# Kernel tuning notes

Measured on AMD Instinct MI355X. Metric: run time of the kernel, lower is better.

Reference implementation:

```python
import jax, jax.numpy as jnp
import numpy as np

N, IN_DIM, OUT_DIM = 8192, 512, 256
ALPHA = 0.2  # LeakyReLU negative slope
MASK_VAL = -9e15


def setup_inputs() -> dict:
    key = jax.random.key(0)
    k1, k2, k3, k4 = jax.random.split(key, 4)
    inp = jax.random.normal(k1, (N, IN_DIM), dtype=jnp.float32)
    adj = jax.random.randint(k2, (N, N), 0, 2, dtype=jnp.int32)
    # xavier-ish scaled params
    weight = jax.random.normal(k3, (IN_DIM, OUT_DIM), dtype=jnp.float32) * (2.0 / (IN_DIM + OUT_DIM)) ** 0.5
    a = jax.random.normal(k4, (2 * OUT_DIM, 1), dtype=jnp.float32) * (2.0 / (2 * OUT_DIM + 1)) ** 0.5
    return {"input": inp, "adj": adj, "weight": weight, "a": a}


def reference(input, adj, weight, a):
    Wh = input @ weight                        # [N, D_out]
    Wh1 = Wh @ a[:OUT_DIM, :]                  # [N, 1]
    Wh2 = Wh @ a[OUT_DIM:, :]                  # [N, 1]
    e = Wh1 + Wh2.T                            # [N, N] broadcast additive score
    e = jnp.where(e > 0, e, ALPHA * e)         # LeakyReLU
    e = jnp.where(adj > 0, e, MASK_VAL)        # adjacency mask
    attention = jax.nn.softmax(e, axis=-1)     # [N, N]
    # dropout p=0.0 -> identity
    out = attention @ Wh                       # [N, D_out]
    return jax.nn.elu(out)
```

## Files before the change

### kernel.cpp

```cpp
#include <hip/hip_runtime.h>
#include <hip/hip_bf16.h>
#include <stdint.h>

#define NN 8192
#define DIN 512
#define DOUT 256
#define NSPLIT 8
#define STRIP (NN / NSPLIT)
#define NSTEP (STRIP / 32)
#define LOG2E 1.4426950408889634f

typedef short short8 __attribute__((ext_vector_type(8)));
typedef float floatx4 __attribute__((ext_vector_type(4)));

__device__ __forceinline__ unsigned short f2bf_rne(float x) {
  unsigned u = __float_as_uint(x);
  u += 0x7fffu + ((u >> 16) & 1u);
  return (unsigned short)(u >> 16);
}

__device__ __forceinline__ unsigned cvt_pk_bf16(float lo, float hi) {
  unsigned r;
  asm("v_cvt_pk_bf16_f32 %0, %1, %2" : "=v"(r) : "v"(lo), "v"(hi));
  return r;
}

__global__ __launch_bounds__(256) void kt_transpose(const float* __restrict__ Wg,
                                                    unsigned short* __restrict__ WT) {
  __shared__ unsigned short sm[32][33];
  int tid = threadIdx.x;
  int bk = blockIdx.x >> 3;
  int bn = blockIdx.x & 7;
  int k0 = bk * 32, n0 = bn * 32;
  int r = tid >> 3, c4 = (tid & 7) * 4;
  const float* src = Wg + (size_t)(k0 + r) * DOUT + n0 + c4;
#pragma unroll
  for (int x = 0; x < 4; ++x) sm[r][c4 + x] = f2bf_rne(src[x]);
  __syncthreads();
  unsigned short* dst = WT + (size_t)(n0 + r) * DIN + k0 + c4;
#pragma unroll
  for (int x = 0; x < 4; ++x) dst[x] = sm[c4 + x][r];
}

__global__ __launch_bounds__(256) void kt_cvtx(const float* __restrict__ X,
                                               unsigned short* __restrict__ Xb) {
  int g = blockIdx.x * 256 + threadIdx.x;
  const float4* p = (const float4*)(X + (size_t)g * 8);
  float4 a = p[0], b = p[1];
  union { unsigned u[4]; short8 s8; } r;
  r.u[0] = cvt_pk_bf16(a.x, a.y);
  r.u[1] = cvt_pk_bf16(a.z, a.w);
  r.u[2] = cvt_pk_bf16(b.x, b.y);
  r.u[3] = cvt_pk_bf16(b.z, b.w);
  *(short8*)(Xb + (size_t)g * 8) = r.s8;
}

__global__ __launch_bounds__(256) void kt_gemm1(const unsigned short* __restrict__ Xb,
                                                const unsigned short* __restrict__ WT,
                                                const float* __restrict__ Ab,
                                                unsigned short* __restrict__ WhT,
                                                float* __restrict__ Wh1,
                                                float* __restrict__ Wh2) {
  int tid = threadIdx.x;
  int w = tid >> 6, lane = tid & 63;
  int col = lane & 15, q = lane >> 4;
  int ib = blockIdx.x & 127;
  int db = blockIdx.x >> 7;
  int i0 = ib * 64;
  int drow = db * 64 + w * 16 + col;
  const unsigned short* abase = WT + (size_t)drow * DIN + q * 8;
  const unsigned short* xbase = Xb + (size_t)(i0 + col) * DIN + q * 8;
  floatx4 acc[4];
#pragma unroll
  for (int t = 0; t < 4; ++t) acc[t] = (floatx4)(0.0f);
  for (int k0 = 0; k0 < DIN; k0 += 32) {
    short8 af = *(const short8*)(abase + k0);
#pragma unroll
    for (int t = 0; t < 4; ++t) {
      short8 bf = *(const short8*)(xbase + (size_t)t * 16 * DIN + k0);
      acc[t] = __builtin_amdgcn_mfma_f32_16x16x32_bf16(af, bf, acc[t], 0, 0, 0);
    }
  }
  int dq = db * 64 + w * 16 + q * 4;
  float a1v[4], a2v[4];
#pragma unroll
  for (int r = 0; r < 4; ++r) {
    a1v[r] = Ab[dq + r] * LOG2E;
    a2v[r] = Ab[DOUT + dq + r] * LOG2E;
  }
#pragma unroll
  for (int t = 0; t < 4; ++t) {
    floatx4 v = acc[t];
    int icol = i0 + t * 16 + col;
#pragma unroll
    for (int r = 0; r < 4; ++r) WhT[(size_t)(dq + r) * NN + icol] = f2bf_rne(v[r]);
    float p1 = v[0] * a1v[0] + v[1] * a1v[1] + v[2] * a1v[2] + v[3] * a1v[3];
    float p2 = v[0] * a2v[0] + v[1] * a2v[1] + v[2] * a2v[2] + v[3] * a2v[3];
    p1 += __shfl_xor(p1, 16);
    p1 += __shfl_xor(p1, 32);
    p2 += __shfl_xor(p2, 16);
    p2 += __shfl_xor(p2, 32);
    if (q == 0) {
      atomicAdd(&Wh1[icol], p1);
      atomicAdd(&Wh2[icol], p2);
    }
  }
}

__device__ __forceinline__ short8 build_a(int4 pa, int4 pb, float wh1, floatx4 w2a,
                                          floatx4 w2b, float& lsum) {
  int av[8] = {pa.x, pa.y, pa.z, pa.w, pb.x, pb.y, pb.z, pb.w};
  float w2[8] = {w2a[0], w2a[1], w2a[2], w2a[3], w2b[0], w2b[1], w2b[2], w2b[3]};
  float wv[8];
#pragma unroll
  for (int e = 0; e < 8; ++e) {
    float sc = wh1 + w2[e];
    sc = fmaxf(sc, 0.2f * sc);
    float ex = __builtin_amdgcn_exp2f(sc);
    wv[e] = (av[e] != 0) ? ex : 0.0f;
  }
  union { unsigned u[4]; short8 s8; } r;
#pragma unroll
  for (int p = 0; p < 4; ++p) {
    unsigned pk = cvt_pk_bf16(wv[2 * p], wv[2 * p + 1]);
    r.u[p] = pk;
    lsum += __uint_as_float(pk << 16) + __uint_as_float(pk & 0xffff0000u);
  }
  return r.s8;
}

__global__ __launch_bounds__(256, 2) void kt_attn(const int* __restrict__ adj,
                                                  const unsigned short* __restrict__ WhT,
                                                  const float* __restrict__ Wh1,
                                                  const float* __restrict__ Wh2,
                                                  float* __restrict__ accg,
                                                  float* __restrict__ lg) {
  __shared__ __align__(16) unsigned short tileB[2][DOUT * 32];
  int tid = threadIdx.x;
  int w = tid >> 6, lane = tid & 63;
  int col = lane & 15, q = lane >> 4;
  int s = blockIdx.x & (NSPLIT - 1);
  int ib = blockIdx.x >> 3;
  int i0 = ib * 128;
  int jb = s * STRIP;

  int r0 = i0 + w * 32 + col;
  float wh1r0 = Wh1[r0];
  float wh1r1 = Wh1[r0 + 16];

  int fsw = (tid >> 1) & 3;
  const unsigned short* gsrc = WhT + (size_t)tid * NN + jb;
  unsigned short* lrow0 = &tileB[0][tid * 32];

  int fc = (col >> 1) & 3;
  const unsigned short* bb0 = &tileB[0][col * 32 + ((q ^ fc) * 8)];

  const int* aptr0 = adj + ((size_t)r0 << 13) + jb + q * 8;
  const int* aptr1 = adj + ((size_t)(r0 + 16) << 13) + jb + q * 8;
  const float* wp = Wh2 + jb + q * 8;

  floatx4 acc0[16], acc1[16];
#pragma unroll
  for (int t = 0; t < 16; ++t) {
    acc0[t] = (floatx4)(0.0f);
    acc1[t] = (floatx4)(0.0f);
  }
  float lp0 = 0.f, lp1 = 0.f;

  short8 st[4];
#pragma unroll
  for (int m = 0; m < 4; ++m) st[m] = *(const short8*)(gsrc + m * 8);
  int4 a0a = *(const int4*)aptr0;
  int4 a0b = *(const int4*)(aptr0 + 4);
  int4 a1a = *(const int4*)aptr1;
  int4 a1b = *(const int4*)(aptr1 + 4);
  floatx4 w2a = *(const floatx4*)wp;
  floatx4 w2b = *(const floatx4*)(wp + 4);

#pragma unroll 1
  for (int k = 0; k < NSTEP; ++k) {
    int bsel = (k & 1) * (DOUT * 32);
    unsigned short* lw = lrow0 + bsel;
#pragma unroll
    for (int m = 0; m < 4; ++m) *(short8*)(lw + ((m ^ fsw) * 8)) = st[m];
    __syncthreads();
    if (k + 1 < NSTEP) {
      const unsigned short* gs = gsrc + (size_t)(k + 1) * 32;
#pragma unroll
      for (int m = 0; m < 4; ++m) st[m] = *(const short8*)(gs + m * 8);
    }
    short8 af0 = build_a(a0a, a0b, wh1r0, w2a, w2b, lp0);
    short8 af1 = build_a(a1a, a1b, wh1r1, w2a, w2b, lp1);
    if (k + 1 < NSTEP) {
      int jn = (k + 1) * 32;
      a0a = *(const int4*)(aptr0 + jn);
      a0b = *(const int4*)(aptr0 + jn + 4);
      a1a = *(const int4*)(aptr1 + jn);
      a1b = *(const int4*)(aptr1 + jn + 4);
      w2a = *(const floatx4*)(wp + jn);
      w2b = *(const floatx4*)(wp + jn + 4);
    }
    const unsigned short* br = bb0 + bsel;
#pragma unroll
    for (int h = 0; h < 4; ++h) {
      short8 bf[4];
#pragma unroll
      for (int t = 0; t < 4; ++t) bf[t] = *(const short8*)(br + (h * 4 + t) * 512);
#pragma unroll
      for (int t = 0; t < 4; ++t) {
        acc0[h * 4 + t] =
            __builtin_amdgcn_mfma_f32_16x16x32_bf16(af0, bf[t], acc0[h * 4 + t], 0, 0, 0);
        acc1[h * 4 + t] =
            __builtin_amdgcn_mfma_f32_16x16x32_bf16(af1, bf[t], acc1[h * 4 + t], 0, 0, 0);
      }
    }
  }

  lp0 += __shfl_xor(lp0, 16);
  lp0 += __shfl_xor(lp0, 32);
  lp1 += __shfl_xor(lp1, 16);
  lp1 += __shfl_xor(lp1, 32);
  if (lane < 16) {
    atomicAdd(&lg[i0 + w * 32 + lane], lp0);
    atomicAdd(&lg[i0 + w * 32 + 16 + lane], lp1);
  }
#pragma unroll
  for (int T = 0; T < 16; ++T) {
    floatx4 v0 = acc0[T];
    floatx4 v1 = acc1[T];
    int dcol = T * 16 + col;
    int irow0 = i0 + w * 32 + q * 4;
#pragma unroll
    for (int r = 0; r < 4; ++r) atomicAdd(&accg[(size_t)(irow0 + r) * DOUT + dcol], v0[r]);
#pragma unroll
    for (int r = 0; r < 4; ++r)
      atomicAdd(&accg[(size_t)(irow0 + 16 + r) * DOUT + dcol], v1[r]);
  }
}

__global__ __launch_bounds__(256) void kt_merge(const float* __restrict__ accg,
                                                const float* __restrict__ lg,
                                                float* __restrict__ out) {
  int g = blockIdx.x * 256 + threadIdx.x;
  int i = g >> 6;
  float inv = 1.0f / lg[i];
  float4 v = *(const float4*)(accg + (size_t)g * 4);
  float o[4] = {v.x * inv, v.y * inv, v.z * inv, v.w * inv};
#pragma unroll
  for (int r = 0; r < 4; ++r) o[r] = o[r] > 0.f ? o[r] : (__expf(o[r]) - 1.f);
  *(float4*)(out + (size_t)g * 4) = make_float4(o[0], o[1], o[2], o[3]);
}

extern "C" void kernel_launch(void* const* d_in, const int* in_sizes, int n_in,
                              void* d_out, int out_size, void* d_ws, size_t ws_size,
                              hipStream_t stream) {
  const float* X = (const float*)d_in[0];
  const int* adj = (const int*)d_in[1];
  const float* Wg = (const float*)d_in[2];
  const float* Ab = (const float*)d_in[3];
  float* out = (float*)d_out;

  char* ws = (char*)d_ws;
  float* accg = (float*)ws;
  unsigned short* Xb = (unsigned short*)ws;
  size_t off = (size_t)NN * DOUT * 4;
  float* lg = (float*)(ws + off);
  off += (size_t)NN * 4;
  float* Wh1 = (float*)(ws + off);
  off += (size_t)NN * 4;
  float* Wh2 = (float*)(ws + off);
  off += (size_t)NN * 4;
  unsigned short* WT = (unsigned short*)(ws + off);
  off += (size_t)DOUT * DIN * 2;
  unsigned short* WhT = (unsigned short*)(ws + off);
  off += (size_t)DOUT * NN * 2;

  hipMemsetAsync(Wh1, 0, (size_t)NN * 8, stream);
  kt_cvtx<<<2048, 256, 0, stream>>>(X, Xb);
  kt_transpose<<<128, 256, 0, stream>>>(Wg, WT);
  kt_gemm1<<<512, 256, 0, stream>>>(Xb, WT, Ab, WhT, Wh1, Wh2);
  hipMemsetAsync(ws, 0, (size_t)NN * DOUT * 4 + (size_t)NN * 4, stream);
  kt_attn<<<(NN / 128) * NSPLIT, 256, 0, stream>>>(adj, WhT, Wh1, Wh2, accg, lg);
  kt_merge<<<2048, 256, 0, stream>>>(accg, lg, out);
}
```

Measured before the change: 471.0 us.

## Load Wh B-fragments directly from global, drop LDS staging, nontemporal adj loads

Removes the double-buffered shared-memory tile for WhT and the per-step __syncthreads. Each wave now loads its 16 B fragments straight from global memory, relying on L2/L1 to serve the four waves that share them. The adjacency loads become nontemporal so the streaming int32 mask does not evict reused data from cache. The cost is four times more global/L1 traffic for the B operand and less latency hiding, since the B loads are issued in the same iteration they are consumed.

```diff
diff --git a/kernel.cpp b/kernel.cpp
--- a/kernel.cpp
+++ b/kernel.cpp
@@ -12,6 +12,7 @@
 
 typedef short short8 __attribute__((ext_vector_type(8)));
 typedef float floatx4 __attribute__((ext_vector_type(4)));
+typedef int intx4 __attribute__((ext_vector_type(4)));
 
 __device__ __forceinline__ unsigned short f2bf_rne(float x) {
   unsigned u = __float_as_uint(x);
@@ -23,6 +24,10 @@
   unsigned r;
   asm("v_cvt_pk_bf16_f32 %0, %1, %2" : "=v"(r) : "v"(lo), "v"(hi));
   return r;
+}
+
+__device__ __forceinline__ intx4 ntld(const int* p) {
+  return __builtin_nontemporal_load((const intx4*)p);
 }
 
 __global__ __launch_bounds__(256) void kt_transpose(const float* __restrict__ Wg,
@@ -107,9 +112,9 @@
   }
 }
 
-__device__ __forceinline__ short8 build_a(int4 pa, int4 pb, float wh1, floatx4 w2a,
+__device__ __forceinline__ short8 build_a(intx4 pa, intx4 pb, float wh1, floatx4 w2a,
                                           floatx4 w2b, float& lsum) {
-  int av[8] = {pa.x, pa.y, pa.z, pa.w, pb.x, pb.y, pb.z, pb.w};
+  int av[8] = {pa[0], pa[1], pa[2], pa[3], pb[0], pb[1], pb[2], pb[3]};
   float w2[8] = {w2a[0], w2a[1], w2a[2], w2a[3], w2b[0], w2b[1], w2b[2], w2b[3]};
   float wv[8];
 #pragma unroll
@@ -135,7 +140,6 @@
                                                   const float* __restrict__ Wh2,
                                                   float* __restrict__ accg,
                                                   float* __restrict__ lg) {
-  __shared__ __align__(16) unsigned short tileB[2][DOUT * 32];
   int tid = threadIdx.x;
   int w = tid >> 6, lane = tid & 63;
   int col = lane & 15, q = lane >> 4;
@@ -148,12 +152,7 @@
   float wh1r0 = Wh1[r0];
   float wh1r1 = Wh1[r0 + 16];
 
-  int fsw = (tid >> 1) & 3;
-  const unsigned short* gsrc = WhT + (size_t)tid * NN + jb;
-  unsigned short* lrow0 = &tileB[0][tid * 32];
-
-  int fc = (col >> 1) & 3;
-  const unsigned short* bb0 = &tileB[0][col * 32 + ((q ^ fc) * 8)];
+  const unsigned short* wbase = WhT + (size_t)col * NN + jb + q * 8;
 
   const int* aptr0 = adj + ((size_t)r0 << 13) + jb + q * 8;
   const int* aptr1 = adj + ((size_t)(r0 + 16) << 13) + jb + q * 8;
@@ -167,52 +166,35 @@
   }
   float lp0 = 0.f, lp1 = 0.f;
 
-  short8 st[4];
-#pragma unroll
-  for (int m = 0; m < 4; ++m) st[m] = *(const short8*)(gsrc + m * 8);
-  int4 a0a = *(const int4*)aptr0;
-  int4 a0b = *(const int4*)(aptr0 + 4);
-  int4 a1a = *(const int4*)aptr1;
-  int4 a1b = *(const int4*)(aptr1 + 4);
+  intx4 a0a = ntld(aptr0);
+  intx4 a0b = ntld(aptr0 + 4);
+  intx4 a1a = ntld(aptr1);
+  intx4 a1b = ntld(aptr1 + 4);
   floatx4 w2a = *(const floatx4*)wp;
   floatx4 w2b = *(const floatx4*)(wp + 4);
 
 #pragma unroll 1
   for (int k = 0; k < NSTEP; ++k) {
-    int bsel = (k & 1) * (DOUT * 32);
-    unsigned short* lw = lrow0 + bsel;
-#pragma unroll
-    for (int m = 0; m < 4; ++m) *(short8*)(lw + ((m ^ fsw) * 8)) = st[m];
-    __syncthreads();
-    if (k + 1 < NSTEP) {
-      const unsigned short* gs = gsrc + (size_t)(k + 1) * 32;
-#pragma unroll
-      for (int m = 0; m < 4; ++m) st[m] = *(const short8*)(gs + m * 8);
-    }
+    int jl = k * 32;
+    short8 bf[16];
+#pragma unroll
+    for (int t = 0; t < 16; ++t)
+      bf[t] = *(const short8*)(wbase + (size_t)t * 16 * NN + jl);
     short8 af0 = build_a(a0a, a0b, wh1r0, w2a, w2b, lp0);
     short8 af1 = build_a(a1a, a1b, wh1r1, w2a, w2b, lp1);
     if (k + 1 < NSTEP) {
-      int jn = (k + 1) * 32;
-      a0a = *(const int4*)(aptr0 + jn);
-      a0b = *(const int4*)(aptr0 + jn + 4);
-      a1a = *(const int4*)(aptr1 + jn);
-      a1b = *(const int4*)(aptr1 + jn + 4);
+      int jn = jl + 32;
+      a0a = ntld(aptr0 + jn);
+      a0b = ntld(aptr0 + jn + 4);
+      a1a = ntld(aptr1 + jn);
+      a1b = ntld(aptr1 + jn + 4);
       w2a = *(const floatx4*)(wp + jn);
       w2b = *(const floatx4*)(wp + jn + 4);
     }
-    const unsigned short* br = bb0 + bsel;
-#pragma unroll
-    for (int h = 0; h < 4; ++h) {
-      short8 bf[4];
-#pragma unroll
-      for (int t = 0; t < 4; ++t) bf[t] = *(const short8*)(br + (h * 4 + t) * 512);
-#pragma unroll
-      for (int t = 0; t < 4; ++t) {
-        acc0[h * 4 + t] =
-            __builtin_amdgcn_mfma_f32_16x16x32_bf16(af0, bf[t], acc0[h * 4 + t], 0, 0, 0);
-        acc1[h * 4 + t] =
-            __builtin_amdgcn_mfma_f32_16x16x32_bf16(af1, bf[t], acc1[h * 4 + t], 0, 0, 0);
-      }
+#pragma unroll
+    for (int t = 0; t < 16; ++t) {
+      acc0[t] = __builtin_amdgcn_mfma_f32_16x16x32_bf16(af0, bf[t], acc0[t], 0, 0, 0);
+      acc1[t] = __builtin_amdgcn_mfma_f32_16x16x32_bf16(af1, bf[t], acc1[t], 0, 0, 0);
     }
   }
 
```

New measurement: 538.3 us. 1.14x slower.

## Stage X tile in swizzled LDS for gemm1 and hand-place attn barrier

Applied to the files above, without the earlier changes.

In the first GEMM, the 64x512 bf16 X tile is loaded into shared memory once, with an XOR swizzle, and the 16 A fragments are preloaded into registers. Previously every wave reread X from global memory on each k step. In the attention kernel, the __syncthreads is replaced by an inline s_waitcnt/s_barrier placed after the next-tile global loads are issued, so those loads are in flight across the barrier. The change costs 64KB of LDS per block in gemm1, which limits occupancy, and uses a hand-written barrier that relies on lgkmcnt covering the LDS writes.

```diff
diff --git a/kernel.cpp b/kernel.cpp
--- a/kernel.cpp
+++ b/kernel.cpp
@@ -55,32 +55,60 @@
   *(short8*)(Xb + (size_t)g * 8) = r.s8;
 }
 
-__global__ __launch_bounds__(256) void kt_gemm1(const unsigned short* __restrict__ Xb,
-                                                const unsigned short* __restrict__ WT,
-                                                const float* __restrict__ Ab,
-                                                unsigned short* __restrict__ WhT,
-                                                float* __restrict__ Wh1,
-                                                float* __restrict__ Wh2) {
+__global__ __launch_bounds__(256, 2) void kt_gemm1(const unsigned short* __restrict__ Xb,
+                                                   const unsigned short* __restrict__ WT,
+                                                   const float* __restrict__ Ab,
+                                                   unsigned short* __restrict__ WhT,
+                                                   float* __restrict__ Wh1,
+                                                   float* __restrict__ Wh2) {
+  __shared__ __align__(16) unsigned short xs[64 * DIN];
   int tid = threadIdx.x;
   int w = tid >> 6, lane = tid & 63;
   int col = lane & 15, q = lane >> 4;
   int ib = blockIdx.x & 127;
   int db = blockIdx.x >> 7;
   int i0 = ib * 64;
+
+  int sr = tid >> 2, sc = tid & 3, sxor = sr & 7;
+  const unsigned short* gX = Xb + (size_t)(i0 + sr) * DIN + sc * 8;
+  unsigned short* lX = xs + sr * DIN;
+  short8 stg[8];
+#pragma unroll
+  for (int n = 0; n < 8; ++n) stg[n] = *(const short8*)(gX + n * 32);
+#pragma unroll
+  for (int n = 0; n < 8; ++n) {
+    int l = sc + n * 4;
+    *(short8*)(lX + ((l ^ sxor) * 8)) = stg[n];
+  }
+#pragma unroll
+  for (int n = 8; n < 16; ++n) stg[n - 8] = *(const short8*)(gX + n * 32);
+#pragma unroll
+  for (int n = 8; n < 16; ++n) {
+    int l = sc + n * 4;
+    *(short8*)(lX + ((l ^ sxor) * 8)) = stg[n - 8];
+  }
+
   int drow = db * 64 + w * 16 + col;
   const unsigned short* abase = WT + (size_t)drow * DIN + q * 8;
-  const unsigned short* xbase = Xb + (size_t)(i0 + col) * DIN + q * 8;
+  short8 af[16];
+#pragma unroll
+  for (int s = 0; s < 16; ++s) af[s] = *(const short8*)(abase + s * 32);
+
+  __syncthreads();
+
   floatx4 acc[4];
 #pragma unroll
   for (int t = 0; t < 4; ++t) acc[t] = (floatx4)(0.0f);
-  for (int k0 = 0; k0 < DIN; k0 += 32) {
-    short8 af = *(const short8*)(abase + k0);
+  int cx = col & 7;
+#pragma unroll
+  for (int s = 0; s < 16; ++s) {
 #pragma unroll
     for (int t = 0; t < 4; ++t) {
-      short8 bf = *(const short8*)(xbase + (size_t)t * 16 * DIN + k0);
-      acc[t] = __builtin_amdgcn_mfma_f32_16x16x32_bf16(af, bf, acc[t], 0, 0, 0);
-    }
-  }
+      short8 bf = *(const short8*)(xs + (t * 16 + col) * DIN + (((s * 4 + q) ^ cx) * 8));
+      acc[t] = __builtin_amdgcn_mfma_f32_16x16x32_bf16(af[s], bf, acc[t], 0, 0, 0);
+    }
+  }
+
   int dq = db * 64 + w * 16 + q * 4;
   float a1v[4], a2v[4];
 #pragma unroll
@@ -143,22 +171,17 @@
   int ib = blockIdx.x >> 3;
   int i0 = ib * 128;
   int jb = s * STRIP;
-
   int r0 = i0 + w * 32 + col;
   float wh1r0 = Wh1[r0];
   float wh1r1 = Wh1[r0 + 16];
-
   int fsw = (tid >> 1) & 3;
   const unsigned short* gsrc = WhT + (size_t)tid * NN + jb;
   unsigned short* lrow0 = &tileB[0][tid * 32];
-
   int fc = (col >> 1) & 3;
   const unsigned short* bb0 = &tileB[0][col * 32 + ((q ^ fc) * 8)];
-
   const int* aptr0 = adj + ((size_t)r0 << 13) + jb + q * 8;
   const int* aptr1 = adj + ((size_t)(r0 + 16) << 13) + jb + q * 8;
   const float* wp = Wh2 + jb + q * 8;
-
   floatx4 acc0[16], acc1[16];
 #pragma unroll
   for (int t = 0; t < 16; ++t) {
@@ -166,7 +189,6 @@
     acc1[t] = (floatx4)(0.0f);
   }
   float lp0 = 0.f, lp1 = 0.f;
-
   short8 st[4];
 #pragma unroll
   for (int m = 0; m < 4; ++m) st[m] = *(const short8*)(gsrc + m * 8);
@@ -176,19 +198,18 @@
   int4 a1b = *(const int4*)(aptr1 + 4);
   floatx4 w2a = *(const floatx4*)wp;
   floatx4 w2b = *(const floatx4*)(wp + 4);
-
 #pragma unroll 1
   for (int k = 0; k < NSTEP; ++k) {
     int bsel = (k & 1) * (DOUT * 32);
     unsigned short* lw = lrow0 + bsel;
 #pragma unroll
     for (int m = 0; m < 4; ++m) *(short8*)(lw + ((m ^ fsw) * 8)) = st[m];
-    __syncthreads();
     if (k + 1 < NSTEP) {
       const unsigned short* gs = gsrc + (size_t)(k + 1) * 32;
 #pragma unroll
       for (int m = 0; m < 4; ++m) st[m] = *(const short8*)(gs + m * 8);
     }
+    asm volatile("s_waitcnt lgkmcnt(0)\ns_barrier" ::: "memory");
     short8 af0 = build_a(a0a, a0b, wh1r0, w2a, w2b, lp0);
     short8 af1 = build_a(a1a, a1b, wh1r1, w2a, w2b, lp1);
     if (k + 1 < NSTEP) {
@@ -200,12 +221,11 @@
       w2a = *(const floatx4*)(wp + jn);
       w2b = *(const floatx4*)(wp + jn + 4);
     }
-    const unsigned short* br = bb0 + bsel;
 #pragma unroll
     for (int h = 0; h < 4; ++h) {
       short8 bf[4];
 #pragma unroll
-      for (int t = 0; t < 4; ++t) bf[t] = *(const short8*)(br + (h * 4 + t) * 512);
+      for (int t = 0; t < 4; ++t) bf[t] = *(const short8*)(bb0 + bsel + (h * 4 + t) * 512);
 #pragma unroll
       for (int t = 0; t < 4; ++t) {
         acc0[h * 4 + t] =
@@ -215,7 +235,6 @@
       }
     }
   }
-
   lp0 += __shfl_xor(lp0, 16);
   lp0 += __shfl_xor(lp0, 32);
   lp1 += __shfl_xor(lp1, 16);
```

New measurement: 461.0 us. -2.1%, faster.
